# Optimization experiments

Hardware: AMD Instinct MI355X
Metric: run time of the kernel (lower is better)

## Reference

```python
import jax, jax.numpy as jnp
import numpy as np

H = 8          # num_heads (in_channels > 8)
BN_EPS = 1e-5  # torch BatchNorm2d default


def _l2norm(w):
    # torch.norm(w, 2, dim=-2, keepdim=True) + 1e-4
    return jnp.sqrt(jnp.sum(w * w, axis=-2, keepdims=True)) + 1e-4


def setup_inputs() -> dict:
    key = jax.random.key(0)
    ks = jax.random.split(key, 6)
    N, C, T, V = 64, 128, 128, 25
    x = jax.random.normal(ks[0], (N, C, T, V), dtype=jnp.float32)
    fc1 = jax.random.normal(ks[1], (3, H, V, V), dtype=jnp.float32)
    rpe = jax.random.normal(ks[2], (3, H, V), dtype=jnp.float32)
    hops = jax.random.randint(ks[3], (V, V), 0, V)
    fc2_w = jax.random.normal(ks[4], (3, C, C // H), dtype=jnp.float32) * 0.1
    fc2_b = jax.random.normal(ks[5], (3, C), dtype=jnp.float32) * 0.1
    gamma = jnp.ones((C,), dtype=jnp.float32)
    beta = jnp.zeros((C,), dtype=jnp.float32)
    return {"x": x, "fc1": fc1, "rpe": rpe, "hops": hops,
            "fc2_w": fc2_w, "fc2_b": fc2_b, "gamma": gamma, "beta": beta}


def reference(x, fc1, rpe, hops, fc2_w, fc2_b, gamma, beta):
    N, C, T, V = x.shape
    c = C // H
    # relative-position embedding gathered by hop distance: (3, H, V, V)
    pos_emb = rpe[:, :, hops]
    x_in = x.reshape(N, H, c, T, V)
    y = jnp.zeros((N, H, c, T, V), dtype=x.dtype)
    for i in range(3):
        # normalized adaptive adjacency + normalized positional term
        w1 = fc1[i] / _l2norm(fc1[i]) + pos_emb[i] / _l2norm(pos_emb[i])  # (H, V, V)
        z = jnp.einsum('nhctv,hvw->nhctw', x_in, w1)
        # grouped 1x1 conv == per-head channel mixing
        wg = fc2_w[i].reshape(H, c, c)                       # (H, out_per_group, in_per_group)
        z = jnp.einsum('nhctv,hdc->nhdtv', z, wg)
        z = z + fc2_b[i].reshape(1, H, c, 1, 1)
        y = y + z
    y = y.reshape(N, C, T, V)
    # BatchNorm2d (training-mode batch statistics, biased variance)
    mean = jnp.mean(y, axis=(0, 2, 3), keepdims=True)
    var = jnp.var(y, axis=(0, 2, 3), keepdims=True)
    y = gamma.reshape(1, C, 1, 1) * (y - mean) * jax.lax.rsqrt(var + BN_EPS) + beta.reshape(1, C, 1, 1)
    # residual (in_channels == out_channels -> identity down) + ReLU
    return jax.nn.relu(y + x)
```

## Files before the change

kernel.cpp:

```cpp
#include <hip/hip_runtime.h>
#include <hip/hip_bf16.h>

namespace {

constexpr int kN = 64, kC = 128, kT = 128, kV = 25, kH = 8, kc = 16;
constexpr int kKS = 13;
constexpr int kBCol = 448;
constexpr int kBStep = kBCol * 32;
constexpr int kXRow = 416;

typedef __attribute__((ext_vector_type(8))) short bf16x8;
typedef __attribute__((ext_vector_type(8))) unsigned short u16x8;
typedef __attribute__((ext_vector_type(4))) float f32x4;

__device__ inline unsigned short f2bf(float f) {
    unsigned int u = __builtin_bit_cast(unsigned int, f);
    u += 0x7fffu + ((u >> 16) & 1u);
    return (unsigned short)(u >> 16);
}
__device__ inline float bf2f(unsigned short s) {
    return __builtin_bit_cast(float, ((unsigned int)s) << 16);
}
__device__ inline void glds16(const void* g, void* l) {
    __builtin_amdgcn_global_load_lds(
        (const __attribute__((address_space(1))) void*)g,
        (__attribute__((address_space(3))) void*)l, 16, 0, 0);
}

__global__ void precompute_w1(const float* __restrict__ fc1,
                              const float* __restrict__ rpe,
                              const int* __restrict__ hops,
                              float* __restrict__ W1) {
    int ih = blockIdx.x;
    int w = threadIdx.x;
    if (w >= kV) return;
    const float* f = fc1 + ih * kV * kV;
    const float* r = rpe + ih * kV;
    float s1 = 0.f, s2 = 0.f;
    for (int v = 0; v < kV; ++v) {
        float a = f[v * kV + w];
        float p = r[hops[v * kV + w]];
        s1 += a * a; s2 += p * p;
    }
    float n1 = sqrtf(s1) + 1e-4f, n2 = sqrtf(s2) + 1e-4f;
    float* o = W1 + ih * kV * kV;
    for (int v = 0; v < kV; ++v) {
        float a = f[v * kV + w];
        float p = r[hops[v * kV + w]];
        o[v * kV + w] = a / n1 + p / n2;
    }
}

__global__ void precompute_W(const float* __restrict__ W1,
                             const float* __restrict__ fc2_w,
                             unsigned short* __restrict__ Wt3) {
    int k = blockIdx.x;
    int h = blockIdx.y;
    unsigned short* outp = Wt3 + ((size_t)h * kKS + k) * kBStep;
    for (int e = threadIdx.x; e < kBStep; e += 256) {
        int col = e >> 5, lo = e & 31;
        int kap = k * 32 + lo;
        int c = kap / 26, vv = kap - c * 26;
        float val = 0.f;
        if (vv < 25 && col < 400) {
            int d = col / 25, w = col - d * 25;
            #pragma unroll
            for (int i = 0; i < 3; ++i) {
                float wg = fc2_w[(i * kC + h * kc + d) * kc + c];
                float w1 = W1[((i * kH + h) * kV + vv) * kV + w];
                val += wg * w1;
            }
        }
        outp[e] = f2bf(val);
    }
}

__global__ __launch_bounds__(256, 2) void gemm_y(const float* __restrict__ x,
                                                 const unsigned short* __restrict__ Wt3,
                                                 unsigned short* __restrict__ yb,
                                                 float2* __restrict__ Pbuf) {
    __shared__ __align__(16) unsigned short Xl[64 * kXRow];
    __shared__ __align__(16) float bounce[6400];

    const int tb = blockIdx.x, n = blockIdx.y, h = blockIdx.z;
    const int tid = threadIdx.x, lane = tid & 63, wv = tid >> 6;
    const int ll = lane & 15, lh = lane >> 4;
    const int t0 = tb * 64;

    const float* xbase = x + ((size_t)(n * kC + h * kc) * kT + t0) * kV;
    const unsigned short* bbase = Wt3 + (size_t)h * kKS * kBStep
                                + ((size_t)(wv * 7) * 16 + ll) * 32 + lh * 8;

    for (int s = 0; s < 4; ++s) {
        #pragma unroll
        for (int q = 0; q < 7; ++q) {
            int e = q * 256 + tid;
            if (e < 1600) {
                int c = e / 400, off = e - c * 400;
                glds16(xbase + (size_t)(s * 4 + c) * 3200 + off * 4,
                       (char*)bounce + (size_t)e * 16);
            }
        }
        __syncthreads();
        {
            const int t = lane, t13 = t % 13;
            const float* bp = bounce + wv * 1600 + t * 25;
            unsigned int* xw = (unsigned int*)&Xl[0] + t * (kXRow / 2) + (s * 4 + wv) * 13;
            #pragma unroll
            for (int i = 0; i < 13; ++i) {
                int p = i + t13; if (p >= 13) p -= 13;
                float f0 = bp[2 * p];
                float f1 = (p < 12) ? bp[2 * p + 1] : 0.f;
                xw[p] = (unsigned)f2bf(f0) | ((unsigned)f2bf(f1) << 16);
            }
        }
        __syncthreads();
    }

    f32x4 acc[4][7];
    #pragma unroll
    for (int a = 0; a < 4; ++a)
        #pragma unroll
        for (int b = 0; b < 7; ++b) acc[a][b] = (f32x4)(0.f);

    auto bld = [&](int k, int ci) -> bf16x8 {
        return *(const bf16x8*)(bbase + (size_t)k * kBStep + ci * 512);
    };
    auto amfma = [&](int k, bf16x8* bf) {
        bf16x8 a0 = *(const bf16x8*)&Xl[(size_t)(0 * 16 + ll) * kXRow + k * 32 + lh * 8];
        bf16x8 a1 = *(const bf16x8*)&Xl[(size_t)(1 * 16 + ll) * kXRow + k * 32 + lh * 8];
        bf16x8 a2 = *(const bf16x8*)&Xl[(size_t)(2 * 16 + ll) * kXRow + k * 32 + lh * 8];
        bf16x8 a3 = *(const bf16x8*)&Xl[(size_t)(3 * 16 + ll) * kXRow + k * 32 + lh * 8];
        #pragma unroll
        for (int ci = 0; ci < 7; ++ci) {
            acc[0][ci] = __builtin_amdgcn_mfma_f32_16x16x32_bf16(a0, bf[ci], acc[0][ci], 0, 0, 0);
            acc[1][ci] = __builtin_amdgcn_mfma_f32_16x16x32_bf16(a1, bf[ci], acc[1][ci], 0, 0, 0);
            acc[2][ci] = __builtin_amdgcn_mfma_f32_16x16x32_bf16(a2, bf[ci], acc[2][ci], 0, 0, 0);
            acc[3][ci] = __builtin_amdgcn_mfma_f32_16x16x32_bf16(a3, bf[ci], acc[3][ci], 0, 0, 0);
        }
    };

    bf16x8 bA[7], bB[7];
    #pragma unroll
    for (int ci = 0; ci < 7; ++ci) bA[ci] = bld(0, ci);

    int k = 0;
    #pragma unroll 1
    for (int it = 0; it < 6; ++it, k += 2) {
        #pragma unroll
        for (int ci = 0; ci < 7; ++ci) bB[ci] = bld(k + 1, ci);
        amfma(k, bA);
        #pragma unroll
        for (int ci = 0; ci < 7; ++ci) bA[ci] = bld(k + 2, ci);
        amfma(k + 1, bB);
    }
    amfma(12, bA);

    #pragma unroll
    for (int rf = 0; rf < 4; ++rf) {
        int t = t0 + rf * 16 + lh * 4;
        #pragma unroll
        for (int ci = 0; ci < 7; ++ci) {
            int m = wv * 112 + ci * 16 + ll;
            if (m < 400) {
                int d = m / 25, w = m - d * 25;
                unsigned short* yp = yb + ((size_t)(n * kC + h * kc + d) * kT + t) * kV + w;
                #pragma unroll
                for (int r = 0; r < 4; ++r)
                    yp[(size_t)r * kV] = f2bf(acc[rf][ci][r]);
            }
        }
    }

    float2* Bs = (float2*)&bounce[0];
    #pragma unroll
    for (int ci = 0; ci < 7; ++ci) {
        float s = 0.f, ss = 0.f;
        #pragma unroll
        for (int rf = 0; rf < 4; ++rf)
            #pragma unroll
            for (int r = 0; r < 4; ++r) {
                float v = acc[rf][ci][r];
                s += v; ss += v * v;
            }
        s  += __shfl_xor(s, 16);  ss += __shfl_xor(ss, 16);
        s  += __shfl_xor(s, 32);  ss += __shfl_xor(ss, 32);
        if (lh == 0) Bs[wv * 112 + ci * 16 + ll] = make_float2(s, ss);
    }
    __syncthreads();
    if (tid < 16) {
        float s = 0.f, ss = 0.f;
        for (int w = 0; w < 25; ++w) {
            float2 p = Bs[tid * 25 + w];
            s += p.x; ss += p.y;
        }
        size_t bid = (size_t)tb + 2 * ((size_t)n + 64 * (size_t)h);
        Pbuf[bid * 16 + tid] = make_float2(s, ss);
    }
}

__global__ void bn_finalize(const float2* __restrict__ Pbuf,
                            const float* __restrict__ gamma,
                            const float* __restrict__ beta,
                            float2* __restrict__ scsh) {
    int ch = threadIdx.x;
    if (ch >= kC) return;
    int h = ch >> 4, d = ch & 15;
    float s = 0.f, ss = 0.f;
    for (int j = 0; j < 128; ++j) {
        float2 p = Pbuf[(size_t)(j + 128 * h) * 16 + d];
        s += p.x; ss += p.y;
    }
    const float inv = 1.f / (float)(kN * kT * kV);
    float mean = s * inv;
    float var  = ss * inv - mean * mean;
    float sc = gamma[ch] * rsqrtf(var + 1e-5f);
    scsh[ch] = make_float2(sc, beta[ch] - mean * sc);
}

__global__ void bn_apply(const unsigned short* __restrict__ yb,
                         const float* __restrict__ x,
                         const float2* __restrict__ scsh,
                         float* __restrict__ out) {
    const size_t total8 = (size_t)kN * kC * kT * kV / 8;
    for (size_t i = (size_t)blockIdx.x * blockDim.x + threadIdx.x; i < total8;
         i += (size_t)gridDim.x * blockDim.x) {
        int ch = (int)((i / 400) % kC);
        float2 sc = scsh[ch];
        u16x8 yv = ((const u16x8*)yb)[i];
        f32x4 x0 = ((const f32x4*)x)[i * 2];
        f32x4 x1 = ((const f32x4*)x)[i * 2 + 1];
        f32x4 o0, o1;
        #pragma unroll
        for (int q = 0; q < 4; ++q) {
            o0[q] = fmaxf(bf2f((unsigned short)yv[q]) * sc.x + sc.y + x0[q], 0.f);
            o1[q] = fmaxf(bf2f((unsigned short)yv[q + 4]) * sc.x + sc.y + x1[q], 0.f);
        }
        ((f32x4*)out)[i * 2]     = o0;
        ((f32x4*)out)[i * 2 + 1] = o1;
    }
}

}

extern "C" void kernel_launch(void* const* d_in, const int* in_sizes, int n_in,
                              void* d_out, int out_size, void* d_ws, size_t ws_size,
                              hipStream_t stream) {
    const float* x     = (const float*)d_in[0];
    const float* fc1   = (const float*)d_in[1];
    const float* rpe   = (const float*)d_in[2];
    const int*   hops  = (const int*)d_in[3];
    const float* fc2w  = (const float*)d_in[4];
    const float* gamma = (const float*)d_in[6];
    const float* beta  = (const float*)d_in[7];
    float* out = (float*)d_out;

    char* ws = (char*)d_ws;
    unsigned short* yb   = (unsigned short*)ws;
    float*          W1   = (float*)(ws + 52428800);
    unsigned short* Wt3  = (unsigned short*)(ws + 52494336);
    float2*         Pbuf = (float2*)(ws + 55476224);
    float2*         scsh = (float2*)(ws + 55607296);

    precompute_w1<<<24, 32, 0, stream>>>(fc1, rpe, hops, W1);
    precompute_W<<<dim3(13, 8), 256, 0, stream>>>(W1, fc2w, Wt3);
    gemm_y<<<dim3(2, 64, 8), 256, 0, stream>>>(x, Wt3, yb, Pbuf);
    bn_finalize<<<1, 128, 0, stream>>>(Pbuf, gamma, beta, scsh);
    bn_apply<<<2048, 256, 0, stream>>>(yb, x, scsh, out);
}
```

Before: 134.0 us.

## Pre-pack x to bf16 tiles, stage weights through LDS, write fp32 y to output

Adds a separate pack_x kernel that converts x into bf16 MFMA-ready A tiles in global memory. The GEMM now keeps A fragments in registers, double-buffers the B weight tiles through LDS with padded rows to avoid bank conflicts, and has each wave own 16 time rows across all 28 column tiles. The result is staged in LDS, written as fp32 straight into the output buffer, and bn_apply then updates it in place. This removes the in-kernel transpose and bf16 conversion of x. In exchange it adds an extra pass over x (a full read plus a bf16 write) and more fp32 traffic for y.

```diff
diff --git a/kernel.cpp b/kernel.cpp
--- a/kernel.cpp
+++ b/kernel.cpp
@@ -6,8 +6,9 @@
 constexpr int kN = 64, kC = 128, kT = 128, kV = 25, kH = 8, kc = 16;
 constexpr int kKS = 13;
 constexpr int kBCol = 448;
-constexpr int kBStep = kBCol * 32;
-constexpr int kXRow = 416;
+constexpr int kBRow = 36;
+constexpr int kBStep = kBCol * kBRow;
+constexpr int kAStep = 64 * 32;
 
 typedef __attribute__((ext_vector_type(8))) short bf16x8;
 typedef __attribute__((ext_vector_type(8))) unsigned short u16x8;
@@ -53,149 +54,146 @@
 
 __global__ void precompute_W(const float* __restrict__ W1,
                              const float* __restrict__ fc2_w,
-                             unsigned short* __restrict__ Wt3) {
+                             unsigned short* __restrict__ Wt4) {
     int k = blockIdx.x;
     int h = blockIdx.y;
-    unsigned short* outp = Wt3 + ((size_t)h * kKS + k) * kBStep;
+    unsigned short* outp = Wt4 + ((size_t)h * kKS + k) * kBStep;
     for (int e = threadIdx.x; e < kBStep; e += 256) {
-        int col = e >> 5, lo = e & 31;
-        int kap = k * 32 + lo;
-        int c = kap / 26, vv = kap - c * 26;
+        int col = e / kBRow, lo = e - col * kBRow;
         float val = 0.f;
-        if (vv < 25 && col < 400) {
-            int d = col / 25, w = col - d * 25;
-            #pragma unroll
-            for (int i = 0; i < 3; ++i) {
-                float wg = fc2_w[(i * kC + h * kc + d) * kc + c];
-                float w1 = W1[((i * kH + h) * kV + vv) * kV + w];
-                val += wg * w1;
+        if (lo < 32 && col < 400) {
+            int kap = k * 32 + lo;
+            int c = kap / 26, vv = kap - c * 26;
+            if (vv < 25) {
+                int d = col / 25, w = col - d * 25;
+                #pragma unroll
+                for (int i = 0; i < 3; ++i) {
+                    float wg = fc2_w[(i * kC + h * kc + d) * kc + c];
+                    float w1 = W1[((i * kH + h) * kV + vv) * kV + w];
+                    val += wg * w1;
+                }
             }
         }
         outp[e] = f2bf(val);
     }
 }
 
-__global__ __launch_bounds__(256, 2) void gemm_y(const float* __restrict__ x,
-                                                 const unsigned short* __restrict__ Wt3,
-                                                 unsigned short* __restrict__ yb,
-                                                 float2* __restrict__ Pbuf) {
-    __shared__ __align__(16) unsigned short Xl[64 * kXRow];
-    __shared__ __align__(16) float bounce[6400];
+__global__ void pack_x(const float* __restrict__ x, unsigned int* __restrict__ Xp) {
+    const int total = kN * kH * 2 * kKS * 1024;
+    for (int o = blockIdx.x * blockDim.x + threadIdx.x; o < total;
+         o += gridDim.x * blockDim.x) {
+        int p = o & 15;
+        int t = (o >> 4) & 63;
+        int rb = o >> 10;
+        int k = rb % 13; int rb2 = rb / 13;
+        int tb = rb2 & 1, h = (rb2 >> 1) & 7, n = rb2 >> 4;
+        int kap = k * 32 + 2 * p;
+        int c0 = kap / 26, v0 = kap - c0 * 26;
+        int c1 = (kap + 1) / 26, v1 = (kap + 1) - c1 * 26;
+        const float* xr = x + ((size_t)(n * kC + h * kc) * kT + tb * 64 + t) * kV;
+        unsigned int lo = 0, hi = 0;
+        if (v0 < 25) lo = f2bf(xr[(size_t)c0 * (kT * kV) + v0]);
+        if (v1 < 25) hi = f2bf(xr[(size_t)c1 * (kT * kV) + v1]);
+        Xp[o] = lo | (hi << 16);
+    }
+}
+
+__global__ __launch_bounds__(256, 2) void mm(const unsigned short* __restrict__ Xp,
+                                             const unsigned short* __restrict__ Wt4,
+                                             float* __restrict__ y,
+                                             float2* __restrict__ Pbuf) {
+    __shared__ __align__(16) unsigned short Bl[2][kBStep];
+    __shared__ __align__(16) float2 Bs[4 * kBCol];
 
     const int tb = blockIdx.x, n = blockIdx.y, h = blockIdx.z;
     const int tid = threadIdx.x, lane = tid & 63, wv = tid >> 6;
     const int ll = lane & 15, lh = lane >> 4;
-    const int t0 = tb * 64;
-
-    const float* xbase = x + ((size_t)(n * kC + h * kc) * kT + t0) * kV;
-    const unsigned short* bbase = Wt3 + (size_t)h * kKS * kBStep
-                                + ((size_t)(wv * 7) * 16 + ll) * 32 + lh * 8;
-
-    for (int s = 0; s < 4; ++s) {
-        #pragma unroll
-        for (int q = 0; q < 7; ++q) {
+
+    const unsigned short* abase = Xp + ((size_t)((n * kH + h) * 2 + tb) * kKS) * kAStep
+                                + (size_t)(wv * 16 + ll) * 32 + lh * 8;
+    const unsigned short* bbase = Wt4 + (size_t)h * kKS * kBStep;
+
+    auto stage = [&](int k, int buf) {
+        const unsigned short* src = bbase + (size_t)k * kBStep;
+        #pragma unroll
+        for (int q = 0; q < 8; ++q) {
             int e = q * 256 + tid;
-            if (e < 1600) {
-                int c = e / 400, off = e - c * 400;
-                glds16(xbase + (size_t)(s * 4 + c) * 3200 + off * 4,
-                       (char*)bounce + (size_t)e * 16);
-            }
-        }
+            if (e < 2016) glds16(src + (size_t)e * 8, &Bl[buf][(size_t)e * 8]);
+        }
+    };
+    auto ldA = [&](int k) -> bf16x8 {
+        return *(const bf16x8*)(abase + (size_t)k * kAStep);
+    };
+
+    f32x4 acc[28];
+    #pragma unroll
+    for (int i = 0; i < 28; ++i) acc[i] = (f32x4)(0.f);
+
+    stage(0, 0);
+    bf16x8 aCur = ldA(0), aNxt = {};
+    __syncthreads();
+
+    #pragma unroll 1
+    for (int k = 0; k < kKS; ++k) {
+        const int cur = k & 1;
+        if (k < kKS - 1) { stage(k + 1, cur ^ 1); aNxt = ldA(k + 1); }
+        #pragma unroll
+        for (int ci = 0; ci < 28; ++ci) {
+            bf16x8 bf = *(const bf16x8*)&Bl[cur][(size_t)(ci * 16 + ll) * kBRow + lh * 8];
+            acc[ci] = __builtin_amdgcn_mfma_f32_16x16x32_bf16(aCur, bf, acc[ci], 0, 0, 0);
+        }
+        aCur = aNxt;
         __syncthreads();
-        {
-            const int t = lane, t13 = t % 13;
-            const float* bp = bounce + wv * 1600 + t * 25;
-            unsigned int* xw = (unsigned int*)&Xl[0] + t * (kXRow / 2) + (s * 4 + wv) * 13;
-            #pragma unroll
-            for (int i = 0; i < 13; ++i) {
-                int p = i + t13; if (p >= 13) p -= 13;
-                float f0 = bp[2 * p];
-                float f1 = (p < 12) ? bp[2 * p + 1] : 0.f;
-                xw[p] = (unsigned)f2bf(f0) | ((unsigned)f2bf(f1) << 16);
-            }
-        }
-        __syncthreads();
-    }
-
-    f32x4 acc[4][7];
+    }
+
+    unsigned short* Yl = &Bl[0][0];
     #pragma unroll
-    for (int a = 0; a < 4; ++a)
-        #pragma unroll
-        for (int b = 0; b < 7; ++b) acc[a][b] = (f32x4)(0.f);
-
-    auto bld = [&](int k, int ci) -> bf16x8 {
-        return *(const bf16x8*)(bbase + (size_t)k * kBStep + ci * 512);
-    };
-    auto amfma = [&](int k, bf16x8* bf) {
-        bf16x8 a0 = *(const bf16x8*)&Xl[(size_t)(0 * 16 + ll) * kXRow + k * 32 + lh * 8];
-        bf16x8 a1 = *(const bf16x8*)&Xl[(size_t)(1 * 16 + ll) * kXRow + k * 32 + lh * 8];
-        bf16x8 a2 = *(const bf16x8*)&Xl[(size_t)(2 * 16 + ll) * kXRow + k * 32 + lh * 8];
-        bf16x8 a3 = *(const bf16x8*)&Xl[(size_t)(3 * 16 + ll) * kXRow + k * 32 + lh * 8];
-        #pragma unroll
-        for (int ci = 0; ci < 7; ++ci) {
-            acc[0][ci] = __builtin_amdgcn_mfma_f32_16x16x32_bf16(a0, bf[ci], acc[0][ci], 0, 0, 0);
-            acc[1][ci] = __builtin_amdgcn_mfma_f32_16x16x32_bf16(a1, bf[ci], acc[1][ci], 0, 0, 0);
-            acc[2][ci] = __builtin_amdgcn_mfma_f32_16x16x32_bf16(a2, bf[ci], acc[2][ci], 0, 0, 0);
-            acc[3][ci] = __builtin_amdgcn_mfma_f32_16x16x32_bf16(a3, bf[ci], acc[3][ci], 0, 0, 0);
-        }
-    };
-
-    bf16x8 bA[7], bB[7];
-    #pragma unroll
-    for (int ci = 0; ci < 7; ++ci) bA[ci] = bld(0, ci);
-
-    int k = 0;
-    #pragma unroll 1
-    for (int it = 0; it < 6; ++it, k += 2) {
-        #pragma unroll
-        for (int ci = 0; ci < 7; ++ci) bB[ci] = bld(k + 1, ci);
-        amfma(k, bA);
-        #pragma unroll
-        for (int ci = 0; ci < 7; ++ci) bA[ci] = bld(k + 2, ci);
-        amfma(k + 1, bB);
-    }
-    amfma(12, bA);
-
-    #pragma unroll
-    for (int rf = 0; rf < 4; ++rf) {
-        int t = t0 + rf * 16 + lh * 4;
-        #pragma unroll
-        for (int ci = 0; ci < 7; ++ci) {
-            int m = wv * 112 + ci * 16 + ll;
+    for (int ci = 0; ci < 28; ++ci) {
+        int m = ci * 16 + ll;
+        float s = 0.f, ss = 0.f;
+        #pragma unroll
+        for (int r = 0; r < 4; ++r) {
+            float v = acc[ci][r];
+            s += v; ss += v * v;
             if (m < 400) {
                 int d = m / 25, w = m - d * 25;
-                unsigned short* yp = yb + ((size_t)(n * kC + h * kc + d) * kT + t) * kV + w;
-                #pragma unroll
-                for (int r = 0; r < 4; ++r)
-                    yp[(size_t)r * kV] = f2bf(acc[rf][ci][r]);
-            }
-        }
-    }
-
-    float2* Bs = (float2*)&bounce[0];
-    #pragma unroll
-    for (int ci = 0; ci < 7; ++ci) {
-        float s = 0.f, ss = 0.f;
-        #pragma unroll
-        for (int rf = 0; rf < 4; ++rf)
-            #pragma unroll
-            for (int r = 0; r < 4; ++r) {
-                float v = acc[rf][ci][r];
-                s += v; ss += v * v;
-            }
+                Yl[d * 1600 + (wv * 16 + lh * 4 + r) * 25 + w] = f2bf(v);
+            }
+        }
         s  += __shfl_xor(s, 16);  ss += __shfl_xor(ss, 16);
         s  += __shfl_xor(s, 32);  ss += __shfl_xor(ss, 32);
-        if (lh == 0) Bs[wv * 112 + ci * 16 + ll] = make_float2(s, ss);
+        if (lh == 0) Bs[wv * kBCol + m] = make_float2(s, ss);
     }
     __syncthreads();
+
+    const size_t ybase = ((size_t)(n * kC + h * kc) * kT + tb * 64) * kV;
+    #pragma unroll
+    for (int q = 0; q < 13; ++q) {
+        int e = q * 256 + tid;
+        if (e < 3200) {
+            int d = e / 200, c = e - d * 200;
+            u16x8 vv = *(const u16x8*)&Yl[(size_t)e * 8];
+            f32x4 o0, o1;
+            #pragma unroll
+            for (int j = 0; j < 4; ++j) {
+                o0[j] = bf2f((unsigned short)vv[j]);
+                o1[j] = bf2f((unsigned short)vv[j + 4]);
+            }
+            float* yp = y + ybase + (size_t)d * (kT * kV) + c * 8;
+            *(f32x4*)yp = o0;
+            *(f32x4*)(yp + 4) = o1;
+        }
+    }
+
     if (tid < 16) {
         float s = 0.f, ss = 0.f;
-        for (int w = 0; w < 25; ++w) {
-            float2 p = Bs[tid * 25 + w];
-            s += p.x; ss += p.y;
-        }
-        size_t bid = (size_t)tb + 2 * ((size_t)n + 64 * (size_t)h);
-        Pbuf[bid * 16 + tid] = make_float2(s, ss);
+        for (int w = 0; w < 25; ++w)
+            #pragma unroll
+            for (int u = 0; u < 4; ++u) {
+                float2 p = Bs[u * kBCol + tid * 25 + w];
+                s += p.x; ss += p.y;
+            }
+        Pbuf[(size_t)(tb + 2 * n + 128 * h) * 16 + tid] = make_float2(s, ss);
     }
 }
 
@@ -218,26 +216,20 @@
     scsh[ch] = make_float2(sc, beta[ch] - mean * sc);
 }
 
-__global__ void bn_apply(const unsigned short* __restrict__ yb,
-                         const float* __restrict__ x,
-                         const float2* __restrict__ scsh,
-                         float* __restrict__ out) {
-    const size_t total8 = (size_t)kN * kC * kT * kV / 8;
-    for (size_t i = (size_t)blockIdx.x * blockDim.x + threadIdx.x; i < total8;
+__global__ void bn_apply(float* __restrict__ y, const float* __restrict__ x,
+                         const float2* __restrict__ scsh) {
+    const size_t total4 = (size_t)kN * kC * kT * kV / 4;
+    for (size_t i = (size_t)blockIdx.x * blockDim.x + threadIdx.x; i < total4;
          i += (size_t)gridDim.x * blockDim.x) {
-        int ch = (int)((i / 400) % kC);
+        int ch = (int)((i / 800) % kC);
         float2 sc = scsh[ch];
-        u16x8 yv = ((const u16x8*)yb)[i];
-        f32x4 x0 = ((const f32x4*)x)[i * 2];
-        f32x4 x1 = ((const f32x4*)x)[i * 2 + 1];
-        f32x4 o0, o1;
-        #pragma unroll
-        for (int q = 0; q < 4; ++q) {
-            o0[q] = fmaxf(bf2f((unsigned short)yv[q]) * sc.x + sc.y + x0[q], 0.f);
-            o1[q] = fmaxf(bf2f((unsigned short)yv[q + 4]) * sc.x + sc.y + x1[q], 0.f);
-        }
-        ((f32x4*)out)[i * 2]     = o0;
-        ((f32x4*)out)[i * 2 + 1] = o1;
+        f32x4 yv = ((const f32x4*)y)[i];
+        f32x4 xv = ((const f32x4*)x)[i];
+        f32x4 o;
+        #pragma unroll
+        for (int q = 0; q < 4; ++q)
+            o[q] = fmaxf(yv[q] * sc.x + sc.y + xv[q], 0.f);
+        ((f32x4*)y)[i] = o;
     }
 }
 
@@ -256,15 +248,16 @@
     float* out = (float*)d_out;
 
     char* ws = (char*)d_ws;
-    unsigned short* yb   = (unsigned short*)ws;
-    float*          W1   = (float*)(ws + 52428800);
-    unsigned short* Wt3  = (unsigned short*)(ws + 52494336);
-    float2*         Pbuf = (float2*)(ws + 55476224);
-    float2*         scsh = (float2*)(ws + 55607296);
+    float*          W1   = (float*)ws;
+    unsigned short* Wt4  = (unsigned short*)(ws + 65536);
+    unsigned int*   Xp   = (unsigned int*)(ws + 3420160);
+    float2*         Pbuf = (float2*)(ws + 57946112);
+    float2*         scsh = (float2*)(ws + 58077184);
 
     precompute_w1<<<24, 32, 0, stream>>>(fc1, rpe, hops, W1);
-    precompute_W<<<dim3(13, 8), 256, 0, stream>>>(W1, fc2w, Wt3);
-    gemm_y<<<dim3(2, 64, 8), 256, 0, stream>>>(x, Wt3, yb, Pbuf);
+    precompute_W<<<dim3(13, 8), 256, 0, stream>>>(W1, fc2w, Wt4);
+    pack_x<<<2048, 256, 0, stream>>>(x, Xp);
+    mm<<<dim3(2, 64, 8), 256, 0, stream>>>((const unsigned short*)Xp, Wt4, out, Pbuf);
     bn_finalize<<<1, 128, 0, stream>>>(Pbuf, gamma, beta, scsh);
-    bn_apply<<<2048, 256, 0, stream>>>(yb, x, scsh, out);
-}
+    bn_apply<<<2048, 256, 0, stream>>>(out, x, scsh);
+}
```

Result: slower. 185.9 us (+38.7%).

## Retile gemm_y into smaller tiles with LDS double-buffered B staging

Applied to the files above, without the earlier changes.

The GEMM grid is retiled from 2x64x8 blocks of 64 time rows and 400 output columns to 4x64x16 blocks of 32 rows and 224 columns. The fused weight slab for each k step is staged into padded LDS with async global-to-LDS loads and double buffering, replacing per-wave direct global loads. The X tile is written in a padded k-packed layout, the BN partial-sum indexing is adapted, and bn_finalize now reduces in parallel with 1024 threads. Per-block reuse of A is lower and there is an extra barrier per k step, in exchange for more blocks, fewer accumulators per wave, and coalesced LDS-served B.

```diff
diff --git a/kernel.cpp b/kernel.cpp
--- a/kernel.cpp
+++ b/kernel.cpp
@@ -5,9 +5,9 @@
 
 constexpr int kN = 64, kC = 128, kT = 128, kV = 25, kH = 8, kc = 16;
 constexpr int kKS = 13;
-constexpr int kBCol = 448;
-constexpr int kBStep = kBCol * 32;
-constexpr int kXRow = 416;
+constexpr int kBRow = 36;
+constexpr int kBSlab = 224 * kBRow;
+constexpr int kXRow = 424;
 
 typedef __attribute__((ext_vector_type(8))) short bf16x8;
 typedef __attribute__((ext_vector_type(8))) unsigned short u16x8;
@@ -53,22 +53,26 @@
 
 __global__ void precompute_W(const float* __restrict__ W1,
                              const float* __restrict__ fc2_w,
-                             unsigned short* __restrict__ Wt3) {
-    int k = blockIdx.x;
-    int h = blockIdx.y;
-    unsigned short* outp = Wt3 + ((size_t)h * kKS + k) * kBStep;
-    for (int e = threadIdx.x; e < kBStep; e += 256) {
-        int col = e >> 5, lo = e & 31;
-        int kap = k * 32 + lo;
-        int c = kap / 26, vv = kap - c * 26;
+                             unsigned short* __restrict__ Wt5) {
+    int k   = blockIdx.x;
+    int hcb = blockIdx.y;
+    int h = hcb >> 1, cb = hcb & 1;
+    unsigned short* outp = Wt5 + ((size_t)hcb * kKS + k) * kBSlab;
+    for (int e = threadIdx.x; e < kBSlab; e += 256) {
+        int col = e / kBRow, lo = e - col * kBRow;
+        int m = cb * 224 + col;
         float val = 0.f;
-        if (vv < 25 && col < 400) {
-            int d = col / 25, w = col - d * 25;
-            #pragma unroll
-            for (int i = 0; i < 3; ++i) {
-                float wg = fc2_w[(i * kC + h * kc + d) * kc + c];
-                float w1 = W1[((i * kH + h) * kV + vv) * kV + w];
-                val += wg * w1;
+        if (lo < 32 && m < 400) {
+            int kap = k * 32 + lo;
+            int c = kap / 26, vv = kap - c * 26;
+            if (vv < 25) {
+                int d = m / 25, w = m - d * 25;
+                #pragma unroll
+                for (int i = 0; i < 3; ++i) {
+                    float wg = fc2_w[(i * kC + h * kc + d) * kc + c];
+                    float w1 = W1[((i * kH + h) * kV + vv) * kV + w];
+                    val += wg * w1;
+                }
             }
         }
         outp[e] = f2bf(val);
@@ -76,126 +80,119 @@
 }
 
 __global__ __launch_bounds__(256, 2) void gemm_y(const float* __restrict__ x,
-                                                 const unsigned short* __restrict__ Wt3,
+                                                 const unsigned short* __restrict__ Wt5,
                                                  unsigned short* __restrict__ yb,
                                                  float2* __restrict__ Pbuf) {
-    __shared__ __align__(16) unsigned short Xl[64 * kXRow];
-    __shared__ __align__(16) float bounce[6400];
-
-    const int tb = blockIdx.x, n = blockIdx.y, h = blockIdx.z;
+    __shared__ __align__(16) unsigned short Xl[32 * kXRow];
+    __shared__ __align__(16) unsigned short Bl[2][kBSlab];
+
+    const int tq = blockIdx.x, n = blockIdx.y, hcb = blockIdx.z;
+    const int h = hcb >> 1, cb = hcb & 1;
+    const int t0 = tq * 32;
     const int tid = threadIdx.x, lane = tid & 63, wv = tid >> 6;
+    const int rg = wv >> 1, cg = wv & 1;
     const int ll = lane & 15, lh = lane >> 4;
-    const int t0 = tb * 64;
 
     const float* xbase = x + ((size_t)(n * kC + h * kc) * kT + t0) * kV;
-    const unsigned short* bbase = Wt3 + (size_t)h * kKS * kBStep
-                                + ((size_t)(wv * 7) * 16 + ll) * 32 + lh * 8;
-
+    const unsigned short* bbase = Wt5 + (size_t)hcb * kKS * kBSlab;
+
+    float* bounce = (float*)&Bl[0][0];
     for (int s = 0; s < 4; ++s) {
         #pragma unroll
-        for (int q = 0; q < 7; ++q) {
+        for (int q = 0; q < 4; ++q) {
             int e = q * 256 + tid;
-            if (e < 1600) {
-                int c = e / 400, off = e - c * 400;
+            if (e < 800) {
+                int c = e / 200, off = e - c * 200;
                 glds16(xbase + (size_t)(s * 4 + c) * 3200 + off * 4,
                        (char*)bounce + (size_t)e * 16);
             }
         }
         __syncthreads();
-        {
-            const int t = lane, t13 = t % 13;
-            const float* bp = bounce + wv * 1600 + t * 25;
-            unsigned int* xw = (unsigned int*)&Xl[0] + t * (kXRow / 2) + (s * 4 + wv) * 13;
+        if (tid < 128) {
+            const int c = tid & 3, t = tid >> 2;
+            const float* bp = bounce + c * 800 + t * 25;
+            unsigned int* xw = (unsigned int*)&Xl[0] + t * (kXRow / 2);
+            const int k0 = (s * 4 + c) * 26;
             #pragma unroll
-            for (int i = 0; i < 13; ++i) {
-                int p = i + t13; if (p >= 13) p -= 13;
-                float f0 = bp[2 * p];
-                float f1 = (p < 12) ? bp[2 * p + 1] : 0.f;
-                xw[p] = (unsigned)f2bf(f0) | ((unsigned)f2bf(f1) << 16);
+            for (int p13 = 0; p13 < 13; ++p13) {
+                int vv = 2 * p13;
+                int kap = k0 + vv;
+                int idx = (kap >> 5) * 16 + ((kap & 31) >> 1);
+                float f0 = bp[vv];
+                float f1 = (vv < 24) ? bp[vv + 1] : 0.f;
+                xw[idx] = (unsigned)f2bf(f0) | ((unsigned)f2bf(f1) << 16);
             }
         }
         __syncthreads();
     }
 
-    f32x4 acc[4][7];
+    auto stage = [&](int k, int buf) {
+        const unsigned short* src = bbase + (size_t)k * kBSlab;
+        #pragma unroll
+        for (int q = 0; q < 4; ++q) {
+            int e = q * 256 + tid;
+            if (e < 1008) glds16(src + (size_t)e * 8, &Bl[buf][(size_t)e * 8]);
+        }
+    };
+    stage(0, 0);
+
+    f32x4 acc[7];
     #pragma unroll
-    for (int a = 0; a < 4; ++a)
-        #pragma unroll
-        for (int b = 0; b < 7; ++b) acc[a][b] = (f32x4)(0.f);
-
-    auto bld = [&](int k, int ci) -> bf16x8 {
-        return *(const bf16x8*)(bbase + (size_t)k * kBStep + ci * 512);
-    };
-    auto amfma = [&](int k, bf16x8* bf) {
-        bf16x8 a0 = *(const bf16x8*)&Xl[(size_t)(0 * 16 + ll) * kXRow + k * 32 + lh * 8];
-        bf16x8 a1 = *(const bf16x8*)&Xl[(size_t)(1 * 16 + ll) * kXRow + k * 32 + lh * 8];
-        bf16x8 a2 = *(const bf16x8*)&Xl[(size_t)(2 * 16 + ll) * kXRow + k * 32 + lh * 8];
-        bf16x8 a3 = *(const bf16x8*)&Xl[(size_t)(3 * 16 + ll) * kXRow + k * 32 + lh * 8];
+    for (int i = 0; i < 7; ++i) acc[i] = (f32x4)(0.f);
+    __syncthreads();
+
+    #pragma unroll 1
+    for (int k = 0; k < kKS; ++k) {
+        const int cur = k & 1;
+        if (k < kKS - 1) stage(k + 1, cur ^ 1);
+        bf16x8 af = *(const bf16x8*)&Xl[(size_t)(rg * 16 + ll) * kXRow + k * 32 + lh * 8];
         #pragma unroll
         for (int ci = 0; ci < 7; ++ci) {
-            acc[0][ci] = __builtin_amdgcn_mfma_f32_16x16x32_bf16(a0, bf[ci], acc[0][ci], 0, 0, 0);
-            acc[1][ci] = __builtin_amdgcn_mfma_f32_16x16x32_bf16(a1, bf[ci], acc[1][ci], 0, 0, 0);
-            acc[2][ci] = __builtin_amdgcn_mfma_f32_16x16x32_bf16(a2, bf[ci], acc[2][ci], 0, 0, 0);
-            acc[3][ci] = __builtin_amdgcn_mfma_f32_16x16x32_bf16(a3, bf[ci], acc[3][ci], 0, 0, 0);
-        }
-    };
-
-    bf16x8 bA[7], bB[7];
+            bf16x8 bf = *(const bf16x8*)&Bl[cur][(size_t)((cg * 7 + ci) * 16 + ll) * kBRow + lh * 8];
+            acc[ci] = __builtin_amdgcn_mfma_f32_16x16x32_bf16(af, bf, acc[ci], 0, 0, 0);
+        }
+        __syncthreads();
+    }
+
     #pragma unroll
-    for (int ci = 0; ci < 7; ++ci) bA[ci] = bld(0, ci);
-
-    int k = 0;
-    #pragma unroll 1
-    for (int it = 0; it < 6; ++it, k += 2) {
-        #pragma unroll
-        for (int ci = 0; ci < 7; ++ci) bB[ci] = bld(k + 1, ci);
-        amfma(k, bA);
-        #pragma unroll
-        for (int ci = 0; ci < 7; ++ci) bA[ci] = bld(k + 2, ci);
-        amfma(k + 1, bB);
-    }
-    amfma(12, bA);
-
-    #pragma unroll
-    for (int rf = 0; rf < 4; ++rf) {
-        int t = t0 + rf * 16 + lh * 4;
-        #pragma unroll
-        for (int ci = 0; ci < 7; ++ci) {
-            int m = wv * 112 + ci * 16 + ll;
-            if (m < 400) {
-                int d = m / 25, w = m - d * 25;
-                unsigned short* yp = yb + ((size_t)(n * kC + h * kc + d) * kT + t) * kV + w;
-                #pragma unroll
-                for (int r = 0; r < 4; ++r)
-                    yp[(size_t)r * kV] = f2bf(acc[rf][ci][r]);
-            }
-        }
-    }
-
-    float2* Bs = (float2*)&bounce[0];
+    for (int ci = 0; ci < 7; ++ci) {
+        int m = cb * 224 + cg * 112 + ci * 16 + ll;
+        if (m < 400) {
+            int d = m / 25, w = m - d * 25;
+            unsigned short* yp = yb + ((size_t)(n * kC + h * kc + d) * kT
+                                       + t0 + rg * 16 + lh * 4) * kV + w;
+            #pragma unroll
+            for (int r = 0; r < 4; ++r)
+                yp[(size_t)r * kV] = f2bf(acc[ci][r]);
+        }
+    }
+
+    float2* Bs = (float2*)&Bl[0][0];
     #pragma unroll
     for (int ci = 0; ci < 7; ++ci) {
         float s = 0.f, ss = 0.f;
         #pragma unroll
-        for (int rf = 0; rf < 4; ++rf)
-            #pragma unroll
-            for (int r = 0; r < 4; ++r) {
-                float v = acc[rf][ci][r];
-                s += v; ss += v * v;
-            }
+        for (int r = 0; r < 4; ++r) {
+            float v = acc[ci][r];
+            s += v; ss += v * v;
+        }
         s  += __shfl_xor(s, 16);  ss += __shfl_xor(ss, 16);
         s  += __shfl_xor(s, 32);  ss += __shfl_xor(ss, 32);
-        if (lh == 0) Bs[wv * 112 + ci * 16 + ll] = make_float2(s, ss);
+        if (lh == 0) Bs[rg * 224 + cg * 112 + ci * 16 + ll] = make_float2(s, ss);
     }
     __syncthreads();
     if (tid < 16) {
+        int d = tid;
         float s = 0.f, ss = 0.f;
         for (int w = 0; w < 25; ++w) {
-            float2 p = Bs[tid * 25 + w];
-            s += p.x; ss += p.y;
-        }
-        size_t bid = (size_t)tb + 2 * ((size_t)n + 64 * (size_t)h);
-        Pbuf[bid * 16 + tid] = make_float2(s, ss);
+            int lc = d * 25 + w - cb * 224;
+            if (lc >= 0 && lc < 224) {
+                float2 p0 = Bs[lc], p1 = Bs[224 + lc];
+                s += p0.x + p1.x; ss += p0.y + p1.y;
+            }
+        }
+        size_t bid = ((size_t)hcb * 64 + n) * 4 + tq;
+        Pbuf[bid * 16 + d] = make_float2(s, ss);
     }
 }
 
@@ -203,19 +200,30 @@
                             const float* __restrict__ gamma,
                             const float* __restrict__ beta,
                             float2* __restrict__ scsh) {
-    int ch = threadIdx.x;
-    if (ch >= kC) return;
+    __shared__ float2 red[1024];
+    int tid = threadIdx.x;
+    int ch = tid >> 3, g = tid & 7;
     int h = ch >> 4, d = ch & 15;
     float s = 0.f, ss = 0.f;
-    for (int j = 0; j < 128; ++j) {
-        float2 p = Pbuf[(size_t)(j + 128 * h) * 16 + d];
+    for (int e = g * 64; e < g * 64 + 64; ++e) {
+        int cb = e >> 8, rem = e & 255;
+        int n = rem >> 2, tq = rem & 3;
+        float2 p = Pbuf[(((size_t)(h * 2 + cb) * 64 + n) * 4 + tq) * 16 + d];
         s += p.x; ss += p.y;
     }
-    const float inv = 1.f / (float)(kN * kT * kV);
-    float mean = s * inv;
-    float var  = ss * inv - mean * mean;
-    float sc = gamma[ch] * rsqrtf(var + 1e-5f);
-    scsh[ch] = make_float2(sc, beta[ch] - mean * sc);
+    red[tid] = make_float2(s, ss);
+    __syncthreads();
+    if (g == 0) {
+        for (int j = 1; j < 8; ++j) {
+            float2 p = red[tid + j];
+            s += p.x; ss += p.y;
+        }
+        const float inv = 1.f / (float)(kN * kT * kV);
+        float mean = s * inv;
+        float var  = ss * inv - mean * mean;
+        float sc = gamma[ch] * rsqrtf(var + 1e-5f);
+        scsh[ch] = make_float2(sc, beta[ch] - mean * sc);
+    }
 }
 
 __global__ void bn_apply(const unsigned short* __restrict__ yb,
@@ -258,13 +266,13 @@
     char* ws = (char*)d_ws;
     unsigned short* yb   = (unsigned short*)ws;
     float*          W1   = (float*)(ws + 52428800);
-    unsigned short* Wt3  = (unsigned short*)(ws + 52494336);
-    float2*         Pbuf = (float2*)(ws + 55476224);
-    float2*         scsh = (float2*)(ws + 55607296);
+    unsigned short* Wt5  = (unsigned short*)(ws + 52494336);
+    float2*         Pbuf = (float2*)(ws + 55848960);
+    float2*         scsh = (float2*)(ws + 56373248);
 
     precompute_w1<<<24, 32, 0, stream>>>(fc1, rpe, hops, W1);
-    precompute_W<<<dim3(13, 8), 256, 0, stream>>>(W1, fc2w, Wt3);
-    gemm_y<<<dim3(2, 64, 8), 256, 0, stream>>>(x, Wt3, yb, Pbuf);
-    bn_finalize<<<1, 128, 0, stream>>>(Pbuf, gamma, beta, scsh);
+    precompute_W<<<dim3(13, 16), 256, 0, stream>>>(W1, fc2w, Wt5);
+    gemm_y<<<dim3(4, 64, 16), 256, 0, stream>>>(x, Wt5, yb, Pbuf);
+    bn_finalize<<<1, 1024, 0, stream>>>(Pbuf, gamma, beta, scsh);
     bn_apply<<<2048, 256, 0, stream>>>(yb, x, scsh, out);
 }
```

Result: slower. 221.4 us (+65.2%).
